# Kernel optimization log

Hardware: AMD Instinct MI355X
Metric: run time of the kernel (lower is better)

The kernel has to match this reference:

```python
import jax, jax.numpy as jnp
import numpy as np


def setup_inputs() -> dict:
    key = jax.random.key(0)
    kq, kk, kv = jax.random.split(key, 3)
    B, S, D = 8, 4096, 64
    q = jax.random.normal(kq, (B, S, D), dtype=jnp.float32)
    k = jax.random.normal(kk, (B, S, D), dtype=jnp.float32)
    v = jax.random.normal(kv, (B, S, D), dtype=jnp.float32)
    mask = jnp.ones((B, S), dtype=jnp.float32)
    return {"q": q, "k": k, "v": v, "mask": mask}


def reference(q, k, v, mask):
    # scores: [B, Sq, Sk], scaled by sqrt(D)
    scale = 1.0 / jnp.sqrt(jnp.asarray(q.shape[-1], q.dtype))
    w = jnp.einsum("bqd,bkd->bqk", q, k) * scale
    # softmax over dim=2 (keys axis for rank-3 input)
    w = jax.nn.softmax(w, axis=2)
    x = jnp.einsum("bqk,bkd->bqd", w, v)
    # post-hoc multiplicative mask on outputs
    x = x * mask[..., None]
    return x
```

## Files before the change

kernel.cpp:

```cpp
#include <hip/hip_runtime.h>

typedef __attribute__((ext_vector_type(8))) short short8;
typedef __attribute__((ext_vector_type(4))) float floatx4;
typedef __attribute__((ext_vector_type(4))) unsigned short ushortx4;

#define MFMA_BF16(A, Bv, C) __builtin_amdgcn_mfma_f32_16x16x32_bf16(A, Bv, C, 0, 0, 0)

#if __has_builtin(__builtin_amdgcn_exp2f)
#define EXP2(x) __builtin_amdgcn_exp2f(x)
#else
#define EXP2(x) exp2f(x)
#endif

__device__ __forceinline__ unsigned short f2bf(float f) {
  unsigned int u = __builtin_bit_cast(unsigned int, f);
  u += 0x7FFFu + ((u >> 16) & 1u);
  return (unsigned short)(u >> 16);
}

__global__ __launch_bounds__(256) void convert_qk(
    const float* __restrict__ q, const float* __restrict__ k,
    unsigned short* __restrict__ qb, unsigned short* __restrict__ kb) {
  int blk = blockIdx.x;
  const float* src;
  unsigned short* dst;
  float scale;
  if (blk < 512) { src = q; dst = qb; scale = 0.18033688011112042f; }
  else           { src = k; dst = kb; scale = 1.0f; blk -= 512; }
  size_t base = (size_t)blk * 4096 + threadIdx.x * 4;
#pragma unroll
  for (int i = 0; i < 4; i++) {
    size_t off = base + (size_t)i * 1024;
    floatx4 f = *(const floatx4*)(src + off);
    ushortx4 h;
    h[0] = f2bf(f[0] * scale);
    h[1] = f2bf(f[1] * scale);
    h[2] = f2bf(f[2] * scale);
    h[3] = f2bf(f[3] * scale);
    *(ushortx4*)(dst + off) = h;
  }
}

__global__ __launch_bounds__(256) void transpose_v(
    const float* __restrict__ v, unsigned short* __restrict__ vt) {
  __shared__ float tile[64 * 68];
  int b = blockIdx.x >> 6, si = blockIdx.x & 63;
  int t = threadIdx.x;
  int r = t >> 2, c4 = (t & 3) * 16;
  const float* vp = v + ((size_t)b * 4096 + si * 64 + r) * 64 + c4;
#pragma unroll
  for (int i = 0; i < 4; i++)
    *(floatx4*)(tile + r * 68 + c4 + i * 4) = *(const floatx4*)(vp + i * 4);
  __syncthreads();
  unsigned short* vo = vt + ((size_t)b * 64 + r) * 4096 + si * 64 + c4;
#pragma unroll
  for (int i = 0; i < 4; i++) {
    ushortx4 h;
#pragma unroll
    for (int j = 0; j < 4; j++) h[j] = f2bf(tile[(c4 + i * 4 + j) * 68 + r]);
    *(ushortx4*)(vo + i * 4) = h;
  }
}

__global__ __launch_bounds__(256, 2) void attn(
    const unsigned short* __restrict__ qb, const unsigned short* __restrict__ kb,
    const unsigned short* __restrict__ vt, const float* __restrict__ mask,
    float* __restrict__ out) {
  __shared__ __align__(16) char smem[35328];
  const int tid = threadIdx.x;
  const int wave = tid >> 6, lane = tid & 63;
  const int c = lane & 15, quad = lane >> 4;
  const int b = blockIdx.x & 7, qt = blockIdx.x >> 3;
  const int q0 = qt * 64;

  const unsigned short* qB = qb + (size_t)b * 4096 * 64;
  const unsigned short* kB = kb + (size_t)b * 4096 * 64;
  const unsigned short* vB = vt + (size_t)b * 64 * 4096;

  short8 qf[4][2];
#pragma unroll
  for (int mt = 0; mt < 4; mt++)
#pragma unroll
    for (int ks = 0; ks < 2; ks++)
      qf[mt][ks] = *(const short8*)(qB + (q0 + mt * 16 + c) * 64 + ks * 32 + quad * 8);

  floatx4 o[4][4], ol[4];
#pragma unroll
  for (int mt = 0; mt < 4; mt++) {
    ol[mt] = (floatx4){0.f, 0.f, 0.f, 0.f};
#pragma unroll
    for (int dt = 0; dt < 4; dt++) o[mt][dt] = (floatx4){0.f, 0.f, 0.f, 0.f};
  }

  short8 ones;
#pragma unroll
  for (int j = 0; j < 8; j++) ones[j] = (short)0x3F80;

  char* pbase = smem + wave * 5120;
  char* pw = pbase + quad * 320 + c * 2;
  const char* prd = pbase + c * 80 + quad * 16;

  for (int t = wave; t < 128; t += 4) {
    const int key0 = t * 32;
    short8 kf[2][2], vf[4];
#pragma unroll
    for (int nt = 0; nt < 2; nt++)
#pragma unroll
      for (int ks = 0; ks < 2; ks++)
        kf[nt][ks] = *(const short8*)(kB + (key0 + nt * 16 + c) * 64 + ks * 32 + quad * 8);
#pragma unroll
    for (int dt = 0; dt < 4; dt++)
      vf[dt] = *(const short8*)(vB + (dt * 16 + c) * 4096 + key0 + quad * 8);

#pragma unroll
    for (int mt = 0; mt < 4; mt++)
#pragma unroll
      for (int nt = 0; nt < 2; nt++) {
        floatx4 s = (floatx4){0.f, 0.f, 0.f, 0.f};
        s = MFMA_BF16(qf[mt][0], kf[nt][0], s);
        s = MFMA_BF16(qf[mt][1], kf[nt][1], s);
#pragma unroll
        for (int r = 0; r < 4; r++) {
          float p = EXP2(s[r]);
          *(unsigned short*)(pw + mt * 1280 + r * 80 + nt * 32) = f2bf(p);
        }
      }

#pragma unroll
    for (int mt = 0; mt < 4; mt++) {
      short8 pf = *(const short8*)(prd + mt * 1280);
#pragma unroll
      for (int dt = 0; dt < 4; dt++) o[mt][dt] = MFMA_BF16(pf, vf[dt], o[mt][dt]);
      ol[mt] = MFMA_BF16(pf, ones, ol[mt]);
    }
  }

  __syncthreads();
  float* obuf = (float*)smem;
  float* lbuf = (float*)(smem + 34816);
  const int w2 = wave & 1;
  if (wave < 2) {
#pragma unroll
    for (int mt = 0; mt < 4; mt++) {
#pragma unroll
      for (int dt = 0; dt < 4; dt++)
#pragma unroll
        for (int r = 0; r < 4; r++)
          obuf[w2 * 4352 + (mt * 16 + quad * 4 + r) * 68 + dt * 16 + c] = o[mt][dt][r];
      if (c == 0)
#pragma unroll
        for (int r = 0; r < 4; r++)
          lbuf[w2 * 64 + mt * 16 + quad * 4 + r] = ol[mt][r];
    }
  }
  __syncthreads();
  if (wave >= 2) {
#pragma unroll
    for (int mt = 0; mt < 4; mt++) {
#pragma unroll
      for (int dt = 0; dt < 4; dt++)
#pragma unroll
        for (int r = 0; r < 4; r++)
          obuf[w2 * 4352 + (mt * 16 + quad * 4 + r) * 68 + dt * 16 + c] += o[mt][dt][r];
      if (c == 0)
#pragma unroll
        for (int r = 0; r < 4; r++)
          lbuf[w2 * 64 + mt * 16 + quad * 4 + r] += ol[mt][r];
    }
  }
  __syncthreads();

  const int row = tid >> 2, dg = (tid & 3) * 16;
  float l = lbuf[row] + lbuf[64 + row];
  float sc = mask[b * 4096 + q0 + row] / l;
  float* op = out + ((size_t)b * 4096 + q0 + row) * 64 + dg;
#pragma unroll
  for (int i = 0; i < 4; i++) {
    floatx4 a = *(const floatx4*)(obuf + row * 68 + dg + i * 4);
    floatx4 b2 = *(const floatx4*)(obuf + 4352 + row * 68 + dg + i * 4);
    floatx4 res = (a + b2) * sc;
    *(floatx4*)(op + i * 4) = res;
  }
}

extern "C" void kernel_launch(void* const* d_in, const int* in_sizes, int n_in,
                              void* d_out, int out_size, void* d_ws, size_t ws_size,
                              hipStream_t stream) {
  const float* q = (const float*)d_in[0];
  const float* k = (const float*)d_in[1];
  const float* v = (const float*)d_in[2];
  const float* mask = (const float*)d_in[3];
  unsigned short* qb = (unsigned short*)d_ws;
  unsigned short* kb = qb + 8 * 4096 * 64;
  unsigned short* vt = kb + 8 * 4096 * 64;
  convert_qk<<<1024, 256, 0, stream>>>(q, k, qb, kb);
  transpose_v<<<512, 256, 0, stream>>>(v, vt);
  attn<<<512, 256, 0, stream>>>(qb, kb, vt, mask, (float*)d_out);
}
```

Measured before the change: 143.8 us.

## Fuse K/V prep into one kernel, load Q in-kernel, and double waves per block

Merges the K conversion and V transpose into a single prep kernel and drops the separate Q conversion by converting Q to bf16 directly inside the attention kernel. The attention block grows to 8 waves, each handling 32 query rows over a quarter of the keys, which halves per-wave register state and raises occupancy. The cross-wave reduction now uses LDS atomicAdd into one buffer. P is rounded to bf16 by truncation instead of round-to-nearest. This removes a launch and some memory traffic, in exchange for LDS atomic contention and slightly lower precision.

```diff
diff --git a/kernel.cpp b/kernel.cpp
--- a/kernel.cpp
+++ b/kernel.cpp
@@ -17,76 +17,82 @@
   u += 0x7FFFu + ((u >> 16) & 1u);
   return (unsigned short)(u >> 16);
 }
+__device__ __forceinline__ unsigned short f2bf_trunc(float f) {
+  return (unsigned short)(__builtin_bit_cast(unsigned int, f) >> 16);
+}
 
-__global__ __launch_bounds__(256) void convert_qk(
-    const float* __restrict__ q, const float* __restrict__ k,
-    unsigned short* __restrict__ qb, unsigned short* __restrict__ kb) {
+__global__ __launch_bounds__(256) void prep_kv(
+    const float* __restrict__ k, const float* __restrict__ v,
+    unsigned short* __restrict__ kb, unsigned short* __restrict__ vt) {
+  __shared__ float tile[64 * 68];
   int blk = blockIdx.x;
-  const float* src;
-  unsigned short* dst;
-  float scale;
-  if (blk < 512) { src = q; dst = qb; scale = 0.18033688011112042f; }
-  else           { src = k; dst = kb; scale = 1.0f; blk -= 512; }
-  size_t base = (size_t)blk * 4096 + threadIdx.x * 4;
+  int t = threadIdx.x;
+  if (blk < 512) {
+    size_t base = (size_t)blk * 4096 + t * 4;
 #pragma unroll
-  for (int i = 0; i < 4; i++) {
-    size_t off = base + (size_t)i * 1024;
-    floatx4 f = *(const floatx4*)(src + off);
-    ushortx4 h;
-    h[0] = f2bf(f[0] * scale);
-    h[1] = f2bf(f[1] * scale);
-    h[2] = f2bf(f[2] * scale);
-    h[3] = f2bf(f[3] * scale);
-    *(ushortx4*)(dst + off) = h;
+    for (int i = 0; i < 4; i++) {
+      size_t off = base + (size_t)i * 1024;
+      floatx4 f = *(const floatx4*)(k + off);
+      ushortx4 h;
+      h[0] = f2bf(f[0]); h[1] = f2bf(f[1]); h[2] = f2bf(f[2]); h[3] = f2bf(f[3]);
+      *(ushortx4*)(kb + off) = h;
+    }
+  } else {
+    blk -= 512;
+    int b = blk >> 6, si = blk & 63;
+    int r = t >> 2, c4 = (t & 3) * 16;
+    const float* vp = v + ((size_t)b * 4096 + si * 64 + r) * 64 + c4;
+#pragma unroll
+    for (int i = 0; i < 4; i++)
+      *(floatx4*)(tile + r * 68 + c4 + i * 4) = *(const floatx4*)(vp + i * 4);
+    __syncthreads();
+    unsigned short* vo = vt + ((size_t)b * 64 + r) * 4096 + si * 64 + c4;
+#pragma unroll
+    for (int i = 0; i < 4; i++) {
+      ushortx4 h;
+#pragma unroll
+      for (int j = 0; j < 4; j++) h[j] = f2bf(tile[(c4 + i * 4 + j) * 68 + r]);
+      *(ushortx4*)(vo + i * 4) = h;
+    }
   }
 }
 
-__global__ __launch_bounds__(256) void transpose_v(
-    const float* __restrict__ v, unsigned short* __restrict__ vt) {
-  __shared__ float tile[64 * 68];
-  int b = blockIdx.x >> 6, si = blockIdx.x & 63;
-  int t = threadIdx.x;
-  int r = t >> 2, c4 = (t & 3) * 16;
-  const float* vp = v + ((size_t)b * 4096 + si * 64 + r) * 64 + c4;
-#pragma unroll
-  for (int i = 0; i < 4; i++)
-    *(floatx4*)(tile + r * 68 + c4 + i * 4) = *(const floatx4*)(vp + i * 4);
-  __syncthreads();
-  unsigned short* vo = vt + ((size_t)b * 64 + r) * 4096 + si * 64 + c4;
-#pragma unroll
-  for (int i = 0; i < 4; i++) {
-    ushortx4 h;
-#pragma unroll
-    for (int j = 0; j < 4; j++) h[j] = f2bf(tile[(c4 + i * 4 + j) * 68 + r]);
-    *(ushortx4*)(vo + i * 4) = h;
-  }
-}
-
-__global__ __launch_bounds__(256, 2) void attn(
-    const unsigned short* __restrict__ qb, const unsigned short* __restrict__ kb,
+__global__ __launch_bounds__(512, 4) void attn(
+    const float* __restrict__ q, const unsigned short* __restrict__ kb,
     const unsigned short* __restrict__ vt, const float* __restrict__ mask,
     float* __restrict__ out) {
-  __shared__ __align__(16) char smem[35328];
+  __shared__ __align__(16) char smem[20480];
   const int tid = threadIdx.x;
   const int wave = tid >> 6, lane = tid & 63;
   const int c = lane & 15, quad = lane >> 4;
+  const int qh = wave & 1, kg = wave >> 1;
   const int b = blockIdx.x & 7, qt = blockIdx.x >> 3;
   const int q0 = qt * 64;
 
-  const unsigned short* qB = qb + (size_t)b * 4096 * 64;
   const unsigned short* kB = kb + (size_t)b * 4096 * 64;
   const unsigned short* vB = vt + (size_t)b * 64 * 4096;
 
-  short8 qf[4][2];
+  const float qscale = 0.18033688011112042f;
+  short8 qf[2][2];
 #pragma unroll
-  for (int mt = 0; mt < 4; mt++)
+  for (int mt = 0; mt < 2; mt++)
 #pragma unroll
-    for (int ks = 0; ks < 2; ks++)
-      qf[mt][ks] = *(const short8*)(qB + (q0 + mt * 16 + c) * 64 + ks * 32 + quad * 8);
+    for (int ks = 0; ks < 2; ks++) {
+      const float* qp = q + ((size_t)b * 4096 + q0 + qh * 32 + mt * 16 + c) * 64 + ks * 32 + quad * 8;
+      floatx4 f0 = *(const floatx4*)qp;
+      floatx4 f1 = *(const floatx4*)(qp + 4);
+      short8 s;
+#pragma unroll
+      for (int j = 0; j < 4; j++) {
+        s[j] = (short)f2bf(f0[j] * qscale);
+        s[4 + j] = (short)f2bf(f1[j] * qscale);
+      }
+      qf[mt][ks] = s;
+    }
 
-  floatx4 o[4][4], ol[4];
+  floatx4 o[2][4], ol[2];
 #pragma unroll
-  for (int mt = 0; mt < 4; mt++) {
+  for (int mt = 0; mt < 2; mt++) {
     ol[mt] = (floatx4){0.f, 0.f, 0.f, 0.f};
 #pragma unroll
     for (int dt = 0; dt < 4; dt++) o[mt][dt] = (floatx4){0.f, 0.f, 0.f, 0.f};
@@ -96,11 +102,11 @@
 #pragma unroll
   for (int j = 0; j < 8; j++) ones[j] = (short)0x3F80;
 
-  char* pbase = smem + wave * 5120;
+  char* pbase = smem + wave * 2560;
   char* pw = pbase + quad * 320 + c * 2;
   const char* prd = pbase + c * 80 + quad * 16;
 
-  for (int t = wave; t < 128; t += 4) {
+  for (int t = kg; t < 128; t += 4) {
     const int key0 = t * 32;
     short8 kf[2][2], vf[4];
 #pragma unroll
@@ -113,21 +119,19 @@
       vf[dt] = *(const short8*)(vB + (dt * 16 + c) * 4096 + key0 + quad * 8);
 
 #pragma unroll
-    for (int mt = 0; mt < 4; mt++)
+    for (int mt = 0; mt < 2; mt++)
 #pragma unroll
       for (int nt = 0; nt < 2; nt++) {
         floatx4 s = (floatx4){0.f, 0.f, 0.f, 0.f};
         s = MFMA_BF16(qf[mt][0], kf[nt][0], s);
         s = MFMA_BF16(qf[mt][1], kf[nt][1], s);
 #pragma unroll
-        for (int r = 0; r < 4; r++) {
-          float p = EXP2(s[r]);
-          *(unsigned short*)(pw + mt * 1280 + r * 80 + nt * 32) = f2bf(p);
-        }
+        for (int r = 0; r < 4; r++)
+          *(unsigned short*)(pw + mt * 1280 + r * 80 + nt * 32) = f2bf_trunc(EXP2(s[r]));
       }
 
 #pragma unroll
-    for (int mt = 0; mt < 4; mt++) {
+    for (int mt = 0; mt < 2; mt++) {
       short8 pf = *(const short8*)(prd + mt * 1280);
 #pragma unroll
       for (int dt = 0; dt < 4; dt++) o[mt][dt] = MFMA_BF16(pf, vf[dt], o[mt][dt]);
@@ -137,50 +141,46 @@
 
   __syncthreads();
   float* obuf = (float*)smem;
-  float* lbuf = (float*)(smem + 34816);
-  const int w2 = wave & 1;
-  if (wave < 2) {
+  float* lbuf = (float*)(smem + 17408);
+  const int orow0 = qh * 32;
+  if (kg == 0) {
 #pragma unroll
-    for (int mt = 0; mt < 4; mt++) {
+    for (int mt = 0; mt < 2; mt++) {
 #pragma unroll
       for (int dt = 0; dt < 4; dt++)
 #pragma unroll
         for (int r = 0; r < 4; r++)
-          obuf[w2 * 4352 + (mt * 16 + quad * 4 + r) * 68 + dt * 16 + c] = o[mt][dt][r];
+          obuf[(orow0 + mt * 16 + quad * 4 + r) * 68 + dt * 16 + c] = o[mt][dt][r];
       if (c == 0)
 #pragma unroll
         for (int r = 0; r < 4; r++)
-          lbuf[w2 * 64 + mt * 16 + quad * 4 + r] = ol[mt][r];
+          lbuf[orow0 + mt * 16 + quad * 4 + r] = ol[mt][r];
     }
   }
   __syncthreads();
-  if (wave >= 2) {
+  if (kg != 0) {
 #pragma unroll
-    for (int mt = 0; mt < 4; mt++) {
+    for (int mt = 0; mt < 2; mt++) {
 #pragma unroll
       for (int dt = 0; dt < 4; dt++)
 #pragma unroll
         for (int r = 0; r < 4; r++)
-          obuf[w2 * 4352 + (mt * 16 + quad * 4 + r) * 68 + dt * 16 + c] += o[mt][dt][r];
+          atomicAdd(&obuf[(orow0 + mt * 16 + quad * 4 + r) * 68 + dt * 16 + c], o[mt][dt][r]);
       if (c == 0)
 #pragma unroll
         for (int r = 0; r < 4; r++)
-          lbuf[w2 * 64 + mt * 16 + quad * 4 + r] += ol[mt][r];
+          atomicAdd(&lbuf[orow0 + mt * 16 + quad * 4 + r], ol[mt][r]);
     }
   }
   __syncthreads();
 
-  const int row = tid >> 2, dg = (tid & 3) * 16;
-  float l = lbuf[row] + lbuf[64 + row];
-  float sc = mask[b * 4096 + q0 + row] / l;
+  const int row = tid >> 3, dg = (tid & 7) * 8;
+  float sc = mask[b * 4096 + q0 + row] / lbuf[row];
   float* op = out + ((size_t)b * 4096 + q0 + row) * 64 + dg;
-#pragma unroll
-  for (int i = 0; i < 4; i++) {
-    floatx4 a = *(const floatx4*)(obuf + row * 68 + dg + i * 4);
-    floatx4 b2 = *(const floatx4*)(obuf + 4352 + row * 68 + dg + i * 4);
-    floatx4 res = (a + b2) * sc;
-    *(floatx4*)(op + i * 4) = res;
-  }
+  floatx4 a0 = *(const floatx4*)(obuf + row * 68 + dg);
+  floatx4 a1 = *(const floatx4*)(obuf + row * 68 + dg + 4);
+  *(floatx4*)op = a0 * sc;
+  *(floatx4*)(op + 4) = a1 * sc;
 }
 
 extern "C" void kernel_launch(void* const* d_in, const int* in_sizes, int n_in,
@@ -190,10 +190,8 @@
   const float* k = (const float*)d_in[1];
   const float* v = (const float*)d_in[2];
   const float* mask = (const float*)d_in[3];
-  unsigned short* qb = (unsigned short*)d_ws;
-  unsigned short* kb = qb + 8 * 4096 * 64;
+  unsigned short* kb = (unsigned short*)d_ws;
   unsigned short* vt = kb + 8 * 4096 * 64;
-  convert_qk<<<1024, 256, 0, stream>>>(q, k, qb, kb);
-  transpose_v<<<512, 256, 0, stream>>>(v, vt);
-  attn<<<512, 256, 0, stream>>>(qb, kb, vt, mask, (float*)d_out);
+  prep_kv<<<1024, 256, 0, stream>>>(k, v, kb, vt);
+  attn<<<512, 512, 0, stream>>>(q, kb, vt, mask, (float*)d_out);
 }
```

After: 226.0 us. 1.57x slower.
